# Performance work log

Measured on AMD Instinct MI355X. Metric: run time of the kernel, lower is better.

Reference implementation:

```python
import jax, jax.numpy as jnp
import numpy as np

D_MODEL = 1024
N_STATE = 64
BASEWIDTH = 3
BC_SCALE = (D_MODEL / BASEWIDTH) ** -0.5  # 'mup' mode width_mult**-0.5
RMS_EPS = 1.1920928955078125e-07  # torch.finfo(float32).eps (RMSNorm eps=None default)


def setup_inputs() -> dict:
    key = jax.random.key(0)
    k1, k2, k3, k4 = jax.random.split(key, 4)
    Bsz, L = 4, 2048
    u = jax.random.normal(k1, (Bsz, D_MODEL, L), dtype=jnp.float32)
    A = jax.random.uniform(k2, (N_STATE,), dtype=jnp.float32) * 0.1  # buffer: rand(N)*A_scale
    B = (jax.random.normal(k3, (N_STATE, D_MODEL), dtype=jnp.float32) + 0.1) * BC_SCALE
    C = (jax.random.normal(k4, (N_STATE, D_MODEL), dtype=jnp.float32) + 0.1) * BC_SCALE
    D = jnp.ones((D_MODEL,), dtype=jnp.float32)
    norm_w = jnp.ones((D_MODEL,), dtype=jnp.float32)
    return {"L": L, "u": u, "A": A, "B": B, "C": C, "D": D, "norm_w": norm_w}


def _ssm(u, A, B, C, D, norm_w):
    # u: [b, d, l]
    scale = BC_SCALE  # applied to Bu, Cu in 'mup' hyperparam mode
    Bu = jnp.einsum('nd,bdl->bnl', B, u) * scale  # [b, n, l]
    Cu = jnp.einsum('nd,bdl->bnl', C, u) * scale  # [b, n, l]
    b, d, l = u.shape
    # shifted_delta == 1 (delta path commented out in source), so
    # h_{t} = A * h_{t-1} + Bu[:, :, t] (outer) u[:, :, t]
    h0 = jnp.zeros((b, d, A.shape[0]), dtype=u.dtype)

    def step(h, xs):
        bu_t, cu_t, u_t = xs  # [b,n], [b,n], [b,d]
        h = h * A + u_t[:, :, None] * bu_t[:, None, :]  # [b, d, n]
        y_t = jnp.einsum('bn,bdn->bd', cu_t, h)
        return h, y_t

    xs = (jnp.moveaxis(Bu, 2, 0), jnp.moveaxis(Cu, 2, 0), jnp.moveaxis(u, 2, 0))
    _, y = jax.lax.scan(step, h0, xs)  # y: [l, b, d]
    y = jnp.moveaxis(y, 0, 2).transpose(1, 0, 2) if False else jnp.transpose(y, (1, 2, 0))  # [b, d, l]
    out = y + u * D[None, :, None]
    # RMSNorm over d_model (apply in [b, l, d] layout)
    x = jnp.transpose(out, (0, 2, 1))  # [b, l, d]
    ms = jnp.mean(x * x, axis=-1, keepdims=True)
    x = x * jax.lax.rsqrt(ms + RMS_EPS) * norm_w
    return jnp.transpose(x, (0, 2, 1))  # [b, d, l]


def reference(L, u, A, B, C, D, norm_w):
    del L  # sequence length == u.shape[-1]
    return _ssm(u, A, B, C, D, norm_w)
```

## Files before the change

### kernel.cpp

```cpp
#include <hip/hip_runtime.h>
#include <stdint.h>

#define DM 1024
#define LS 2048
#define RMS_EPS 1.1920928955078125e-07f
#define S2 0.0029296875f

typedef __attribute__((ext_vector_type(8))) short bf16x8;
typedef __attribute__((ext_vector_type(4))) float f32x4;

__device__ __forceinline__ unsigned short f2bf(float f) {
  uint32_t u = __builtin_bit_cast(uint32_t, f);
  u += 0x7FFFu + ((u >> 16) & 1u);
  return (unsigned short)(u >> 16);
}

__global__ __launch_bounds__(256) void k0_prep(const float* __restrict__ B,
                                               const float* __restrict__ C,
                                               unsigned short* __restrict__ Bbf) {
  int i4 = blockIdx.x * 256 + threadIdx.x;
  const float4* src = (i4 < 16384) ? (const float4*)B : (const float4*)C;
  float4 v = src[i4 & 16383];
  ushort4 o;
  o.x = f2bf(v.x); o.y = f2bf(v.y); o.z = f2bf(v.z); o.w = f2bf(v.w);
  ((ushort4*)Bbf)[i4] = o;
}

__global__ __launch_bounds__(256) void k1_gemm(const float* __restrict__ u,
                                               const unsigned short* __restrict__ Bbf,
                                               float* __restrict__ BuCuT) {
  const int b    = blockIdx.y;
  const int l0   = blockIdx.x * 16;
  const int lane = threadIdx.x & 63;
  const int w    = threadIdx.x >> 6;
  const float* ub = u + (size_t)b * DM * LS;

  __shared__ bf16x8 tile[128][16];

  {
    const int lq = lane & 3;
    const int kg = lane >> 2;
    const int kbase = 256 * w + 16 * kg;
    #pragma unroll
    for (int h = 0; h < 2; ++h) {
      float4 vv[8];
      #pragma unroll
      for (int r = 0; r < 8; ++r)
        vv[r] = *(const float4*)(ub + (size_t)(kbase + 8*h + r) * LS + l0 + 4*lq);
      const int k8 = 32*w + 2*kg + h;
      #pragma unroll
      for (int c = 0; c < 4; ++c) {
        union { bf16x8 v; unsigned short s[8]; } t;
        #pragma unroll
        for (int r = 0; r < 8; ++r) t.s[r] = f2bf(((const float*)&vv[r])[c]);
        tile[k8][(4*lq + c) ^ (k8 & 3)] = t.v;
      }
    }
  }
  __syncthreads();

  const int n = lane & 15;
  const int q = lane >> 4;
  f32x4 acc[2] = {};
  #pragma unroll 4
  for (int it = 0; it < 32; ++it) {
    bf16x8 bfrag = tile[4*it + q][n ^ q];
    #pragma unroll
    for (int rt = 0; rt < 2; ++rt) {
      int row = 32*w + 16*rt + n;
      bf16x8 a = *(const bf16x8*)(Bbf + (size_t)row * DM + 32*it + 8*q);
      acc[rt] = __builtin_amdgcn_mfma_f32_16x16x32_bf16(a, bfrag, acc[rt], 0, 0, 0);
    }
  }

  float* ob = BuCuT + (size_t)b * LS * 128;
  #pragma unroll
  for (int rt = 0; rt < 2; ++rt) {
    int col = l0 + n;
    int row = 32*w + 16*rt + 4*q;
    *(f32x4*)(ob + (size_t)col * 128 + row) = acc[rt];
  }
}

__global__ __launch_bounds__(1024) void k23_conv(const float* __restrict__ u,
                                                 const float* __restrict__ BuCuT,
                                                 const float* __restrict__ A,
                                                 const float* __restrict__ Dv,
                                                 const float* __restrict__ nw,
                                                 float* __restrict__ out) {
  const int b   = blockIdx.y;
  const int t0  = blockIdx.x * 16;
  const int tid = threadIdx.x;
  const float* ub = u + (size_t)b * DM * LS;
  float* ob = out + (size_t)b * DM * LS;

  __shared__ float Row[32][132];
  __shared__ float apow[64][17];
  __shared__ float Part[256][20];
  __shared__ float KwS[16][20];
  __shared__ float ss[16][260];
  __shared__ float rsq[16];

  {
    const int r  = tid >> 5;
    const int c4 = tid & 31;
    const int g  = t0 - 16 + r;
    float4 v = (g >= 0) ? *(const float4*)(BuCuT + ((size_t)b * LS + g) * 128 + 4*c4)
                        : make_float4(0.f, 0.f, 0.f, 0.f);
    *(float4*)&Row[r][4*c4] = v;
  }
  if (tid < 64) {
    float a = A[tid], p = 1.f;
    #pragma unroll
    for (int j = 0; j < 16; ++j) { apow[tid][j] = p; p *= a; }
  }
  __syncthreads();

  {
    const int t  = tid & 15;
    const int p  = (tid >> 4) & 15;
    const int jq = tid >> 8;
    float4 cu = *(const float4*)&Row[16 + t][64 + 4*p];
    float4 aa = *(const float4*)(A + 4*p);
    float pw[4];
    pw[0] = cu.x * S2 * apow[4*p+0][4*jq];
    pw[1] = cu.y * S2 * apow[4*p+1][4*jq];
    pw[2] = cu.z * S2 * apow[4*p+2][4*jq];
    pw[3] = cu.w * S2 * apow[4*p+3][4*jq];
    #pragma unroll
    for (int jj = 0; jj < 4; ++jj) {
      const int j = 4*jq + jj;
      float4 b4 = *(const float4*)&Row[16 + t - j][4*p];
      float s = pw[0]*b4.x + pw[1]*b4.y + pw[2]*b4.z + pw[3]*b4.w;
      Part[16*j + t][p] = s;
      pw[0] *= aa.x; pw[1] *= aa.y; pw[2] *= aa.z; pw[3] *= aa.w;
    }
  }
  __syncthreads();
  if (tid < 256) {
    float s = 0.f;
    #pragma unroll
    for (int p4 = 0; p4 < 4; ++p4) {
      float4 v = *(const float4*)&Part[tid][4*p4];
      s += (v.x + v.y) + (v.z + v.w);
    }
    KwS[tid & 15][tid >> 4] = s;
  }
  __syncthreads();

  const int tg = tid & 3;
  const int dr = tid >> 2;
  float kw[4][16];
  #pragma unroll
  for (int k = 0; k < 4; ++k)
    #pragma unroll
    for (int i = 0; i < 4; ++i)
      *(float4*)&kw[k][4*i] = *(const float4*)&KwS[4*tg + k][4*i];

  const int cbase = t0 - 16 + 4*tg;
  float y[4][4];
  float ps[4] = {0.f, 0.f, 0.f, 0.f};
  #pragma unroll 1
  for (int c = 0; c < 4; ++c) {
    const int d = dr + 256*c;
    const float* row = ub + (size_t)d * LS;
    float wr[20];
    #pragma unroll
    for (int s5 = 0; s5 < 5; ++s5) {
      int g = cbase + 4*s5;
      float4 v = (g >= 0) ? *(const float4*)(row + g)
                          : make_float4(0.f, 0.f, 0.f, 0.f);
      wr[4*s5+0] = v.x; wr[4*s5+1] = v.y; wr[4*s5+2] = v.z; wr[4*s5+3] = v.w;
    }
    const float Dd = Dv[d];
    #pragma unroll
    for (int k = 0; k < 4; ++k) {
      float acc = wr[16 + k] * Dd;
      #pragma unroll
      for (int j = 0; j < 16; ++j)
        acc = fmaf(kw[k][j], wr[16 + k - j], acc);
      y[c][k] = acc;
      ps[k] = fmaf(acc, acc, ps[k]);
    }
  }

  #pragma unroll
  for (int k = 0; k < 4; ++k) ss[4*tg + k][dr] = ps[k];
  __syncthreads();
  {
    const int w = tid >> 6;
    const int l = tid & 63;
    float s = ss[w][l] + ss[w][l + 64] + ss[w][l + 128] + ss[w][l + 192];
    #pragma unroll
    for (int off = 32; off > 0; off >>= 1) s += __shfl_down(s, off, 64);
    if (l == 0) rsq[w] = rsqrtf(s * (1.f/1024.f) + RMS_EPS);
  }
  __syncthreads();
  float rq[4];
  #pragma unroll
  for (int k = 0; k < 4; ++k) rq[k] = rsq[4*tg + k];
  #pragma unroll
  for (int c = 0; c < 4; ++c) {
    const int d = dr + 256*c;
    const float wn = nw[d];
    float4 o;
    o.x = y[c][0] * rq[0] * wn;
    o.y = y[c][1] * rq[1] * wn;
    o.z = y[c][2] * rq[2] * wn;
    o.w = y[c][3] * rq[3] * wn;
    *(float4*)(ob + (size_t)d * LS + t0 + 4*tg) = o;
  }
}

extern "C" void kernel_launch(void* const* d_in, const int* in_sizes, int n_in,
                              void* d_out, int out_size, void* d_ws, size_t ws_size,
                              hipStream_t stream) {
  const float* u  = (const float*)d_in[1];
  const float* A  = (const float*)d_in[2];
  const float* B  = (const float*)d_in[3];
  const float* C  = (const float*)d_in[4];
  const float* Dv = (const float*)d_in[5];
  const float* nw = (const float*)d_in[6];
  float* out = (float*)d_out;

  float* BuCuT = (float*)d_ws;
  unsigned short* Bbf = (unsigned short*)((char*)d_ws + (4u << 20));

  k0_prep <<<dim3(128),    dim3(256),  0, stream>>>(B, C, Bbf);
  k1_gemm <<<dim3(128, 4), dim3(256),  0, stream>>>(u, Bbf, BuCuT);
  k23_conv<<<dim3(128, 4), dim3(1024), 0, stream>>>(u, BuCuT, A, Dv, nw, out);
}
```

Before: 143.9 us.

## Fuse projection GEMM into conv/RMSNorm kernel, recomputing halo in-block

Merges the bf16 MFMA GEMM computing Bu/Cu into the convolution-plus-RMSNorm kernel, so each block computes its own 32-timestep window of Bu (including a 16-step halo) and 16 steps of Cu in shared memory. This removes the BuCuT workspace round trip through global memory and one kernel launch. The cost is redundant GEMM work and extra u reads for the halo. It also remaps block indices across XCDs, computes A powers by squaring instead of a table, and replaces the RMS partial-sum reduction with wave shuffles.

New measurement: 145.9 us. Within noise of the previous version (+1.4%).

```diff
diff --git a/kernel.cpp b/kernel.cpp
--- a/kernel.cpp
+++ b/kernel.cpp
@@ -26,93 +26,74 @@
   ((ushort4*)Bbf)[i4] = o;
 }
 
-__global__ __launch_bounds__(256) void k1_gemm(const float* __restrict__ u,
-                                               const unsigned short* __restrict__ Bbf,
-                                               float* __restrict__ BuCuT) {
-  const int b    = blockIdx.y;
-  const int l0   = blockIdx.x * 16;
-  const int lane = threadIdx.x & 63;
-  const int w    = threadIdx.x >> 6;
-  const float* ub = u + (size_t)b * DM * LS;
-
-  __shared__ bf16x8 tile[128][16];
-
-  {
-    const int lq = lane & 3;
-    const int kg = lane >> 2;
-    const int kbase = 256 * w + 16 * kg;
-    #pragma unroll
-    for (int h = 0; h < 2; ++h) {
-      float4 vv[8];
-      #pragma unroll
-      for (int r = 0; r < 8; ++r)
-        vv[r] = *(const float4*)(ub + (size_t)(kbase + 8*h + r) * LS + l0 + 4*lq);
-      const int k8 = 32*w + 2*kg + h;
-      #pragma unroll
-      for (int c = 0; c < 4; ++c) {
-        union { bf16x8 v; unsigned short s[8]; } t;
-        #pragma unroll
-        for (int r = 0; r < 8; ++r) t.s[r] = f2bf(((const float*)&vv[r])[c]);
-        tile[k8][(4*lq + c) ^ (k8 & 3)] = t.v;
-      }
-    }
-  }
-  __syncthreads();
-
-  const int n = lane & 15;
-  const int q = lane >> 4;
-  f32x4 acc[2] = {};
-  #pragma unroll 4
-  for (int it = 0; it < 32; ++it) {
-    bf16x8 bfrag = tile[4*it + q][n ^ q];
-    #pragma unroll
-    for (int rt = 0; rt < 2; ++rt) {
-      int row = 32*w + 16*rt + n;
-      bf16x8 a = *(const bf16x8*)(Bbf + (size_t)row * DM + 32*it + 8*q);
-      acc[rt] = __builtin_amdgcn_mfma_f32_16x16x32_bf16(a, bfrag, acc[rt], 0, 0, 0);
-    }
-  }
-
-  float* ob = BuCuT + (size_t)b * LS * 128;
-  #pragma unroll
-  for (int rt = 0; rt < 2; ++rt) {
-    int col = l0 + n;
-    int row = 32*w + 16*rt + 4*q;
-    *(f32x4*)(ob + (size_t)col * 128 + row) = acc[rt];
-  }
-}
-
-__global__ __launch_bounds__(1024) void k23_conv(const float* __restrict__ u,
-                                                 const float* __restrict__ BuCuT,
-                                                 const float* __restrict__ A,
-                                                 const float* __restrict__ Dv,
-                                                 const float* __restrict__ nw,
-                                                 float* __restrict__ out) {
-  const int b   = blockIdx.y;
-  const int t0  = blockIdx.x * 16;
+__global__ __launch_bounds__(1024) void kf(const float* __restrict__ u,
+                                           const unsigned short* __restrict__ Bbf,
+                                           const float* __restrict__ A,
+                                           const float* __restrict__ Dv,
+                                           const float* __restrict__ nw,
+                                           float* __restrict__ out) {
+  const int wg  = blockIdx.x;
+  const int nbx = (wg & 7) * 64 + (wg >> 3);
+  const int b   = nbx >> 7;
+  const int t0  = (nbx & 127) << 4;
   const int tid = threadIdx.x;
+  const int lane = tid & 63;
+  const int w    = tid >> 6;
   const float* ub = u + (size_t)b * DM * LS;
   float* ob = out + (size_t)b * DM * LS;
 
-  __shared__ float Row[32][132];
-  __shared__ float apow[64][17];
-  __shared__ float Part[256][20];
-  __shared__ float KwS[16][20];
-  __shared__ float ss[16][260];
-  __shared__ float rsq[16];
+  __shared__ __align__(16) char SMEM[65536];
+  __shared__ __align__(16) float Bu[32][68];
+  __shared__ __align__(16) float Cu[16][68];
+  bf16x8 (*tile)[32] = (bf16x8 (*)[32])SMEM;
+  float (*Part)[20]  = (float (*)[20])SMEM;
+  float (*KwS)[20]   = (float (*)[20])(SMEM + 20480);
+  float (*SS2)[20]   = (float (*)[20])(SMEM + 21760);
+  float *rsq         = (float*)(SMEM + 23040);
 
   {
-    const int r  = tid >> 5;
-    const int c4 = tid & 31;
-    const int g  = t0 - 16 + r;
-    float4 v = (g >= 0) ? *(const float4*)(BuCuT + ((size_t)b * LS + g) * 128 + 4*c4)
-                        : make_float4(0.f, 0.f, 0.f, 0.f);
-    *(float4*)&Row[r][4*c4] = v;
-  }
-  if (tid < 64) {
-    float a = A[tid], p = 1.f;
-    #pragma unroll
-    for (int j = 0; j < 16; ++j) { apow[tid][j] = p; p *= a; }
+    const int h16 = w >> 3;
+    const int ks  = w & 7;
+    const int tb  = lane >> 5;
+    const int kg  = (lane >> 2) & 7;
+    const int lq  = lane & 3;
+    const int kbase = 128*ks + 64*tb + 8*kg;
+    const int gcol  = t0 - 16 + 16*h16 + 4*lq;
+    float4 vv[8];
+    if (gcol >= 0) {
+      #pragma unroll
+      for (int r = 0; r < 8; ++r)
+        vv[r] = *(const float4*)(ub + (size_t)(kbase + r) * LS + gcol);
+    } else {
+      #pragma unroll
+      for (int r = 0; r < 8; ++r) vv[r] = make_float4(0.f, 0.f, 0.f, 0.f);
+    }
+    const int k8 = 16*ks + 8*tb + kg;
+    #pragma unroll
+    for (int c = 0; c < 4; ++c) {
+      union { bf16x8 v; unsigned short s[8]; } t8;
+      #pragma unroll
+      for (int r = 0; r < 8; ++r) t8.s[r] = f2bf(((const float*)&vv[r])[c]);
+      tile[k8][16*h16 + ((4*lq + c) ^ (k8 & 3))] = t8.v;
+    }
+  }
+  __syncthreads();
+
+  {
+    const int nn = lane & 15, q = lane >> 4;
+    const int wm = w & 7, wn = w >> 3;
+    const unsigned short* arow = Bbf + (size_t)(16*wm + nn) * DM;
+    f32x4 acc = {};
+    #pragma unroll 4
+    for (int it = 0; it < 32; ++it) {
+      bf16x8 bfrag = tile[4*it + q][16*wn + (nn ^ q)];
+      bf16x8 afrag = *(const bf16x8*)(arow + 32*it + 8*q);
+      acc = __builtin_amdgcn_mfma_f32_16x16x32_bf16(afrag, bfrag, acc, 0, 0, 0);
+    }
+    const int ucol = 16*wn + nn;
+    const int bcr  = 16*wm + 4*q;
+    if (wm < 4)       *(f32x4*)&Bu[ucol][bcr]            = acc;
+    else if (wn == 1) *(f32x4*)&Cu[ucol - 16][bcr - 64]  = acc;
   }
   __syncthreads();
 
@@ -120,20 +101,26 @@
     const int t  = tid & 15;
     const int p  = (tid >> 4) & 15;
     const int jq = tid >> 8;
-    float4 cu = *(const float4*)&Row[16 + t][64 + 4*p];
-    float4 aa = *(const float4*)(A + 4*p);
-    float pw[4];
-    pw[0] = cu.x * S2 * apow[4*p+0][4*jq];
-    pw[1] = cu.y * S2 * apow[4*p+1][4*jq];
-    pw[2] = cu.z * S2 * apow[4*p+2][4*jq];
-    pw[3] = cu.w * S2 * apow[4*p+3][4*jq];
+    const float4 cu = *(const float4*)&Cu[t][4*p];
+    const float4 aa = *(const float4*)(A + 4*p);
+    float a2x = aa.x*aa.x, a2y = aa.y*aa.y, a2z = aa.z*aa.z, a2w = aa.w*aa.w;
+    float a4x = a2x*a2x,  a4y = a2y*a2y,  a4z = a2z*a2z,  a4w = a2w*a2w;
+    float a8x = a4x*a4x,  a8y = a4y*a4y,  a8z = a4z*a4z,  a8w = a4w*a4w;
+    float acx = a8x*a4x,  acy = a8y*a4y,  acz = a8z*a4z,  acw = a8w*a4w;
+    float apx = (jq==0)?1.f:(jq==1)?a4x:(jq==2)?a8x:acx;
+    float apy = (jq==0)?1.f:(jq==1)?a4y:(jq==2)?a8y:acy;
+    float apz = (jq==0)?1.f:(jq==1)?a4z:(jq==2)?a8z:acz;
+    float apw = (jq==0)?1.f:(jq==1)?a4w:(jq==2)?a8w:acw;
+    float pw0 = cu.x * S2 * apx;
+    float pw1 = cu.y * S2 * apy;
+    float pw2 = cu.z * S2 * apz;
+    float pw3 = cu.w * S2 * apw;
     #pragma unroll
     for (int jj = 0; jj < 4; ++jj) {
       const int j = 4*jq + jj;
-      float4 b4 = *(const float4*)&Row[16 + t - j][4*p];
-      float s = pw[0]*b4.x + pw[1]*b4.y + pw[2]*b4.z + pw[3]*b4.w;
-      Part[16*j + t][p] = s;
-      pw[0] *= aa.x; pw[1] *= aa.y; pw[2] *= aa.z; pw[3] *= aa.w;
+      const float4 b4 = *(const float4*)&Bu[16 + t - j][4*p];
+      Part[16*j + t][p] = pw0*b4.x + pw1*b4.y + pw2*b4.z + pw3*b4.w;
+      pw0 *= aa.x; pw1 *= aa.y; pw2 *= aa.z; pw3 *= aa.w;
     }
   }
   __syncthreads();
@@ -141,7 +128,7 @@
     float s = 0.f;
     #pragma unroll
     for (int p4 = 0; p4 < 4; ++p4) {
-      float4 v = *(const float4*)&Part[tid][4*p4];
+      const float4 v = *(const float4*)&Part[tid][4*p4];
       s += (v.x + v.y) + (v.z + v.w);
     }
     KwS[tid & 15][tid >> 4] = s;
@@ -183,17 +170,23 @@
       ps[k] = fmaf(acc, acc, ps[k]);
     }
   }
-
-  #pragma unroll
-  for (int k = 0; k < 4; ++k) ss[4*tg + k][dr] = ps[k];
-  __syncthreads();
-  {
-    const int w = tid >> 6;
-    const int l = tid & 63;
-    float s = ss[w][l] + ss[w][l + 64] + ss[w][l + 128] + ss[w][l + 192];
-    #pragma unroll
-    for (int off = 32; off > 0; off >>= 1) s += __shfl_down(s, off, 64);
-    if (l == 0) rsq[w] = rsqrtf(s * (1.f/1024.f) + RMS_EPS);
+  #pragma unroll
+  for (int k = 0; k < 4; ++k) {
+    ps[k] += __shfl_xor(ps[k], 4, 64);
+    ps[k] += __shfl_xor(ps[k], 8, 64);
+    ps[k] += __shfl_xor(ps[k], 16, 64);
+    ps[k] += __shfl_xor(ps[k], 32, 64);
+  }
+  if (lane < 4) {
+    float4 o = make_float4(ps[0], ps[1], ps[2], ps[3]);
+    *(float4*)&SS2[w][4*lane] = o;
+  }
+  __syncthreads();
+  if (tid < 16) {
+    float s = 0.f;
+    #pragma unroll
+    for (int ww = 0; ww < 16; ++ww) s += SS2[ww][tid];
+    rsq[tid] = rsqrtf(s * (1.f/1024.f) + RMS_EPS);
   }
   __syncthreads();
   float rq[4];
@@ -202,12 +195,12 @@
   #pragma unroll
   for (int c = 0; c < 4; ++c) {
     const int d = dr + 256*c;
-    const float wn = nw[d];
+    const float wn2 = nw[d];
     float4 o;
-    o.x = y[c][0] * rq[0] * wn;
-    o.y = y[c][1] * rq[1] * wn;
-    o.z = y[c][2] * rq[2] * wn;
-    o.w = y[c][3] * rq[3] * wn;
+    o.x = y[c][0] * rq[0] * wn2;
+    o.y = y[c][1] * rq[1] * wn2;
+    o.z = y[c][2] * rq[2] * wn2;
+    o.w = y[c][3] * rq[3] * wn2;
     *(float4*)(ob + (size_t)d * LS + t0 + 4*tg) = o;
   }
 }
@@ -223,10 +216,8 @@
   const float* nw = (const float*)d_in[6];
   float* out = (float*)d_out;
 
-  float* BuCuT = (float*)d_ws;
-  unsigned short* Bbf = (unsigned short*)((char*)d_ws + (4u << 20));
-
-  k0_prep <<<dim3(128),    dim3(256),  0, stream>>>(B, C, Bbf);
-  k1_gemm <<<dim3(128, 4), dim3(256),  0, stream>>>(u, Bbf, BuCuT);
-  k23_conv<<<dim3(128, 4), dim3(1024), 0, stream>>>(u, BuCuT, A, Dv, nw, out);
-}
+  unsigned short* Bbf = (unsigned short*)d_ws;
+
+  k0_prep<<<dim3(128), dim3(256),  0, stream>>>(B, C, Bbf);
+  kf     <<<dim3(512), dim3(1024), 0, stream>>>(u, Bbf, A, Dv, nw, out);
+}
```
